# Performance work log

Hardware: AMD Instinct MI355X
Metric: run time of the kernel (lower is better)

## Reference

```python
import jax, jax.numpy as jnp
import numpy as np

B, S, D, Q = 8, 4096, 1024, 16  # batch, seq, embed_dim, n_qubits==ffn_dim


def setup_inputs() -> dict:
    key = jax.random.key(0)
    k = jax.random.split(key, 5)
    x = jax.random.normal(k[0], (B, S, D), dtype=jnp.float32)
    W1 = jax.random.normal(k[1], (D, Q), dtype=jnp.float32) * 0.02
    b1 = jnp.zeros((Q,), dtype=jnp.float32)
    theta = jax.random.normal(k[2], (Q,), dtype=jnp.float32)
    W2 = jax.random.normal(k[3], (Q, D), dtype=jnp.float32) * 0.02
    b2 = jnp.zeros((D,), dtype=jnp.float32)
    return {"x": x, "W1": W1, "b1": b1, "theta": theta, "W2": W2, "b2": b2}


def reference(x, W1, b1, theta, W2, b2):
    # linear1 + ReLU (dropout is identity in eval mode)
    h = jax.nn.relu(jnp.einsum("bsd,dq->bsq", x, W1) + b1)  # [B,S,Q] angles
    # QLayer: RY(h_i) then RY(theta_i) on wire i from |0>; rotations on the
    # same wire compose additively and <Z> after RY(a)|0> is cos(a), so
    # MeasureAll(PauliZ) == cos(h + theta) per wire (exact, product state).
    z = jnp.cos(h + theta)  # [B,S,Q]
    # linear2
    return jnp.einsum("bsq,qd->bsd", z, W2) + b2
```

## Files before the change

kernel.cpp:

```cpp
#include <hip/hip_runtime.h>
#include <math.h>
#include <stdint.h>

#define ROWS_TOTAL 32768
#define DDIM 1024
#define QDIM 16

typedef __attribute__((ext_vector_type(8))) short bf16x8;
typedef __attribute__((ext_vector_type(4))) float f32x4;

union ABfrag { uint32_t u[4]; bf16x8 v; };

__device__ __forceinline__ uint32_t packhi(uint32_t a, uint32_t b) {
  return __builtin_amdgcn_perm(b, a, 0x07060302u);
}

#define ZTPB 512
#define ZWPB 8
#define ZNBLOCKS (ROWS_TOTAL / 16)

__global__ __launch_bounds__(ZTPB, 4)
void z_kernel(const float* __restrict__ x, const float* __restrict__ W1,
              const float* __restrict__ b1, const float* __restrict__ theta,
              float* __restrict__ z, int zstride) {
  const int t    = threadIdx.x;
  const int lane = t & 63;
  const int wid  = t >> 6;
  const int g    = lane >> 4;
  const int q5   = lane & 15;

  __shared__ __align__(16) float xs[16][DDIM];
  __shared__ __align__(16) float red[ZWPB][64][4];

  const int row0 = blockIdx.x * 16;
  const int kb   = wid * 128;

  const float bq = b1[q5];
  const float tq = theta[q5];

  float wf[4][8];
#pragma unroll
  for (int s = 0; s < 4; ++s) {
    const float* wp = W1 + (size_t)(kb + 32 * s + 4 * g) * QDIM + q5;
#pragma unroll
    for (int j = 0; j < 4; ++j) wf[s][j] = wp[(size_t)j * QDIM];
#pragma unroll
    for (int j = 0; j < 4; ++j) wf[s][4 + j] = wp[(size_t)(16 + j) * QDIM];
  }

  float4 st[8];
  {
    const int rs = 2 * wid;
#pragma unroll
    for (int rr = 0; rr < 2; ++rr) {
      const float* xp = x + (size_t)(row0 + rs + rr) * DDIM;
#pragma unroll
      for (int p = 0; p < 4; ++p)
        st[rr * 4 + p] =
            *reinterpret_cast<const float4*>(xp + 4 * (64 * p + lane));
    }
#pragma unroll
    for (int rr = 0; rr < 2; ++rr) {
      const int r = rs + rr;
#pragma unroll
      for (int p = 0; p < 4; ++p) {
        const int u = 64 * p + lane;
        *reinterpret_cast<float4*>(&xs[r][4 * (u ^ (r & 7))]) =
            st[rr * 4 + p];
      }
    }
  }

  ABfrag bhi[4], blo[4];
#pragma unroll
  for (int s = 0; s < 4; ++s) {
    uint32_t u[8], lo[8];
#pragma unroll
    for (int j = 0; j < 8; ++j) {
      u[j]  = __float_as_uint(wf[s][j]);
      lo[j] = __float_as_uint(wf[s][j] - __uint_as_float(u[j] & 0xFFFF0000u));
    }
    bhi[s].u[0] = packhi(u[0], u[1]);   bhi[s].u[1] = packhi(u[2], u[3]);
    bhi[s].u[2] = packhi(u[4], u[5]);   bhi[s].u[3] = packhi(u[6], u[7]);
    blo[s].u[0] = packhi(lo[0], lo[1]); blo[s].u[1] = packhi(lo[2], lo[3]);
    blo[s].u[2] = packhi(lo[4], lo[5]); blo[s].u[3] = packhi(lo[6], lo[7]);
  }

  __syncthreads();

  const int rr = lane & 15;
  const int ub = 32 * wid;
  float4 a0[4], a1[4];
#pragma unroll
  for (int s = 0; s < 4; ++s) {
    a0[s] = *reinterpret_cast<const float4*>(
        &xs[rr][4 * ((ub + 8 * s + g) ^ (rr & 7))]);
    a1[s] = *reinterpret_cast<const float4*>(
        &xs[rr][4 * ((ub + 8 * s + 4 + g) ^ (rr & 7))]);
  }

  f32x4 acc = {0.f, 0.f, 0.f, 0.f};
#pragma unroll
  for (int s = 0; s < 4; ++s) {
    const float fv[8] = {a0[s].x, a0[s].y, a0[s].z, a0[s].w,
                         a1[s].x, a1[s].y, a1[s].z, a1[s].w};
    uint32_t u[8], lo[8];
#pragma unroll
    for (int j = 0; j < 8; ++j) {
      u[j]  = __float_as_uint(fv[j]);
      lo[j] = __float_as_uint(fv[j] - __uint_as_float(u[j] & 0xFFFF0000u));
    }
    ABfrag ahi, alo;
    ahi.u[0] = packhi(u[0], u[1]);   ahi.u[1] = packhi(u[2], u[3]);
    ahi.u[2] = packhi(u[4], u[5]);   ahi.u[3] = packhi(u[6], u[7]);
    alo.u[0] = packhi(lo[0], lo[1]); alo.u[1] = packhi(lo[2], lo[3]);
    alo.u[2] = packhi(lo[4], lo[5]); alo.u[3] = packhi(lo[6], lo[7]);

    acc = __builtin_amdgcn_mfma_f32_16x16x32_bf16(ahi.v, bhi[s].v, acc, 0, 0, 0);
    acc = __builtin_amdgcn_mfma_f32_16x16x32_bf16(alo.v, bhi[s].v, acc, 0, 0, 0);
    acc = __builtin_amdgcn_mfma_f32_16x16x32_bf16(ahi.v, blo[s].v, acc, 0, 0, 0);
  }

  *reinterpret_cast<f32x4*>(&red[wid][lane][0]) = acc;
  __syncthreads();

  if (wid == 0) {
    f32x4 s0 = *reinterpret_cast<const f32x4*>(&red[0][lane][0]);
#pragma unroll
    for (int w = 1; w < ZWPB; ++w)
      s0 += *reinterpret_cast<const f32x4*>(&red[w][lane][0]);

    const int r0 = g * 4;
#pragma unroll
    for (int i = 0; i < 4; ++i) {
      const float sv = fmaxf(s0[i] + bq, 0.f) + tq;
      z[(size_t)(row0 + r0 + i) * zstride + q5] = __cosf(sv);
    }
  }
}

#define OTPB 256
#define ORPB 16
#define ONBLOCKS (ROWS_TOTAL / ORPB)

__global__ __launch_bounds__(OTPB, 4)
void o_kernel(const float* z, int zstride, const float* __restrict__ W2,
              const float* __restrict__ b2, float* out) {
  const int t   = threadIdx.x;
  const int col = 4 * t;

  float4 w2r[QDIM];
#pragma unroll
  for (int q = 0; q < QDIM; ++q)
    w2r[q] = *reinterpret_cast<const float4*>(W2 + (size_t)q * DDIM + col);
  const float4 bb = *reinterpret_cast<const float4*>(b2 + col);

  const int row0 = blockIdx.x * ORPB;

  const float* zp0 = z + (size_t)row0 * zstride;
  float4 zc0 = *reinterpret_cast<const float4*>(zp0 + 0);
  float4 zc1 = *reinterpret_cast<const float4*>(zp0 + 4);
  float4 zc2 = *reinterpret_cast<const float4*>(zp0 + 8);
  float4 zc3 = *reinterpret_cast<const float4*>(zp0 + 12);

#pragma unroll
  for (int r = 0; r < ORPB; ++r) {
    float4 zn0 = zc0, zn1 = zc1, zn2 = zc2, zn3 = zc3;
    if (r + 1 < ORPB) {
      const float* znp = z + (size_t)(row0 + r + 1) * zstride;
      zn0 = *reinterpret_cast<const float4*>(znp + 0);
      zn1 = *reinterpret_cast<const float4*>(znp + 4);
      zn2 = *reinterpret_cast<const float4*>(znp + 8);
      zn3 = *reinterpret_cast<const float4*>(znp + 12);
    }

    const float zv[16] = {zc0.x, zc0.y, zc0.z, zc0.w,
                          zc1.x, zc1.y, zc1.z, zc1.w,
                          zc2.x, zc2.y, zc2.z, zc2.w,
                          zc3.x, zc3.y, zc3.z, zc3.w};
    float4 acc = bb;
#pragma unroll
    for (int q = 0; q < QDIM; ++q) {
      acc.x = fmaf(zv[q], w2r[q].x, acc.x);
      acc.y = fmaf(zv[q], w2r[q].y, acc.y);
      acc.z = fmaf(zv[q], w2r[q].z, acc.z);
      acc.w = fmaf(zv[q], w2r[q].w, acc.w);
    }
    *reinterpret_cast<float4*>(out + (size_t)(row0 + r) * DDIM + col) = acc;

    zc0 = zn0; zc1 = zn1; zc2 = zn2; zc3 = zn3;
  }
}

extern "C" void kernel_launch(void* const* d_in, const int* in_sizes, int n_in,
                              void* d_out, int out_size, void* d_ws, size_t ws_size,
                              hipStream_t stream) {
  const float* x     = (const float*)d_in[0];
  const float* W1    = (const float*)d_in[1];
  const float* b1    = (const float*)d_in[2];
  const float* theta = (const float*)d_in[3];
  const float* W2    = (const float*)d_in[4];
  const float* b2    = (const float*)d_in[5];
  float* out = (float*)d_out;

  const size_t zbytes = (size_t)ROWS_TOTAL * QDIM * sizeof(float);
  float* zbuf;
  int zstride;
  if (d_ws != nullptr && ws_size >= zbytes) {
    zbuf = (float*)d_ws;
    zstride = QDIM;
  } else {
    zbuf = out;
    zstride = DDIM;
  }

  z_kernel<<<dim3(ZNBLOCKS), dim3(ZTPB), 0, stream>>>(x, W1, b1, theta, zbuf, zstride);
  o_kernel<<<dim3(ONBLOCKS), dim3(OTPB), 0, stream>>>(zbuf, zstride, W2, b2, out);
}
```

Baseline: 52.77 us.

## Fuse z computation and output projection into a single kernel

Merges the two kernels into one: the cosine features for each 16-row tile stay in shared memory and feed the W2 projection inside the same block, with each thread producing two output columns. This removes the global round trip of the intermediate z buffer and one kernel launch. In exchange it adds a block barrier, 32 more registers per thread for W2, and couples the read-heavy and write-heavy phases, so each block's output writes start only after its reduction finishes.

```diff
diff --git a/kernel.cpp b/kernel.cpp
--- a/kernel.cpp
+++ b/kernel.cpp
@@ -15,14 +15,15 @@
   return __builtin_amdgcn_perm(b, a, 0x07060302u);
 }
 
-#define ZTPB 512
-#define ZWPB 8
-#define ZNBLOCKS (ROWS_TOTAL / 16)
+#define TPB 512
+#define WPB 8
+#define NBLOCKS (ROWS_TOTAL / 16)
 
-__global__ __launch_bounds__(ZTPB, 4)
-void z_kernel(const float* __restrict__ x, const float* __restrict__ W1,
-              const float* __restrict__ b1, const float* __restrict__ theta,
-              float* __restrict__ z, int zstride) {
+__global__ __launch_bounds__(TPB, 4)
+void fused_kernel(const float* __restrict__ x, const float* __restrict__ W1,
+                  const float* __restrict__ b1, const float* __restrict__ theta,
+                  const float* __restrict__ W2, const float* __restrict__ b2,
+                  float* __restrict__ out) {
   const int t    = threadIdx.x;
   const int lane = t & 63;
   const int wid  = t >> 6;
@@ -30,7 +31,8 @@
   const int q5   = lane & 15;
 
   __shared__ __align__(16) float xs[16][DDIM];
-  __shared__ __align__(16) float red[ZWPB][64][4];
+  __shared__ __align__(16) float red[WPB][64][4];
+  __shared__ __align__(16) float zs[16][QDIM];
 
   const int row0 = blockIdx.x * 16;
   const int kb   = wid * 128;
@@ -121,74 +123,47 @@
     acc = __builtin_amdgcn_mfma_f32_16x16x32_bf16(ahi.v, blo[s].v, acc, 0, 0, 0);
   }
 
+  float2 w2r[QDIM];
+#pragma unroll
+  for (int q = 0; q < QDIM; ++q)
+    w2r[q] = *reinterpret_cast<const float2*>(W2 + (size_t)q * DDIM + 2 * t);
+  const float2 bb = *reinterpret_cast<const float2*>(b2 + 2 * t);
+
   *reinterpret_cast<f32x4*>(&red[wid][lane][0]) = acc;
   __syncthreads();
 
   if (wid == 0) {
     f32x4 s0 = *reinterpret_cast<const f32x4*>(&red[0][lane][0]);
 #pragma unroll
-    for (int w = 1; w < ZWPB; ++w)
+    for (int w = 1; w < WPB; ++w)
       s0 += *reinterpret_cast<const f32x4*>(&red[w][lane][0]);
 
     const int r0 = g * 4;
 #pragma unroll
     for (int i = 0; i < 4; ++i) {
       const float sv = fmaxf(s0[i] + bq, 0.f) + tq;
-      z[(size_t)(row0 + r0 + i) * zstride + q5] = __cosf(sv);
+      zs[r0 + i][q5] = __cosf(sv);
     }
   }
-}
-
-#define OTPB 256
-#define ORPB 16
-#define ONBLOCKS (ROWS_TOTAL / ORPB)
-
-__global__ __launch_bounds__(OTPB, 4)
-void o_kernel(const float* z, int zstride, const float* __restrict__ W2,
-              const float* __restrict__ b2, float* out) {
-  const int t   = threadIdx.x;
-  const int col = 4 * t;
-
-  float4 w2r[QDIM];
-#pragma unroll
-  for (int q = 0; q < QDIM; ++q)
-    w2r[q] = *reinterpret_cast<const float4*>(W2 + (size_t)q * DDIM + col);
-  const float4 bb = *reinterpret_cast<const float4*>(b2 + col);
-
-  const int row0 = blockIdx.x * ORPB;
-
-  const float* zp0 = z + (size_t)row0 * zstride;
-  float4 zc0 = *reinterpret_cast<const float4*>(zp0 + 0);
-  float4 zc1 = *reinterpret_cast<const float4*>(zp0 + 4);
-  float4 zc2 = *reinterpret_cast<const float4*>(zp0 + 8);
-  float4 zc3 = *reinterpret_cast<const float4*>(zp0 + 12);
+  __syncthreads();
 
 #pragma unroll
-  for (int r = 0; r < ORPB; ++r) {
-    float4 zn0 = zc0, zn1 = zc1, zn2 = zc2, zn3 = zc3;
-    if (r + 1 < ORPB) {
-      const float* znp = z + (size_t)(row0 + r + 1) * zstride;
-      zn0 = *reinterpret_cast<const float4*>(znp + 0);
-      zn1 = *reinterpret_cast<const float4*>(znp + 4);
-      zn2 = *reinterpret_cast<const float4*>(znp + 8);
-      zn3 = *reinterpret_cast<const float4*>(znp + 12);
+  for (int r = 0; r < 16; ++r) {
+    float o0 = bb.x, o1 = bb.y;
+#pragma unroll
+    for (int jb = 0; jb < 4; ++jb) {
+      const float4 zv = *reinterpret_cast<const float4*>(&zs[r][4 * jb]);
+      o0 = fmaf(zv.x, w2r[4 * jb + 0].x, o0);
+      o1 = fmaf(zv.x, w2r[4 * jb + 0].y, o1);
+      o0 = fmaf(zv.y, w2r[4 * jb + 1].x, o0);
+      o1 = fmaf(zv.y, w2r[4 * jb + 1].y, o1);
+      o0 = fmaf(zv.z, w2r[4 * jb + 2].x, o0);
+      o1 = fmaf(zv.z, w2r[4 * jb + 2].y, o1);
+      o0 = fmaf(zv.w, w2r[4 * jb + 3].x, o0);
+      o1 = fmaf(zv.w, w2r[4 * jb + 3].y, o1);
     }
-
-    const float zv[16] = {zc0.x, zc0.y, zc0.z, zc0.w,
-                          zc1.x, zc1.y, zc1.z, zc1.w,
-                          zc2.x, zc2.y, zc2.z, zc2.w,
-                          zc3.x, zc3.y, zc3.z, zc3.w};
-    float4 acc = bb;
-#pragma unroll
-    for (int q = 0; q < QDIM; ++q) {
-      acc.x = fmaf(zv[q], w2r[q].x, acc.x);
-      acc.y = fmaf(zv[q], w2r[q].y, acc.y);
-      acc.z = fmaf(zv[q], w2r[q].z, acc.z);
-      acc.w = fmaf(zv[q], w2r[q].w, acc.w);
-    }
-    *reinterpret_cast<float4*>(out + (size_t)(row0 + r) * DDIM + col) = acc;
-
-    zc0 = zn0; zc1 = zn1; zc2 = zn2; zc3 = zn3;
+    *reinterpret_cast<float2*>(out + (size_t)(row0 + r) * DDIM + 2 * t) =
+        make_float2(o0, o1);
   }
 }
 
@@ -203,17 +178,6 @@
   const float* b2    = (const float*)d_in[5];
   float* out = (float*)d_out;
 
-  const size_t zbytes = (size_t)ROWS_TOTAL * QDIM * sizeof(float);
-  float* zbuf;
-  int zstride;
-  if (d_ws != nullptr && ws_size >= zbytes) {
-    zbuf = (float*)d_ws;
-    zstride = QDIM;
-  } else {
-    zbuf = out;
-    zstride = DDIM;
-  }
-
-  z_kernel<<<dim3(ZNBLOCKS), dim3(ZTPB), 0, stream>>>(x, W1, b1, theta, zbuf, zstride);
-  o_kernel<<<dim3(ONBLOCKS), dim3(OTPB), 0, stream>>>(zbuf, zstride, W2, b2, out);
+  fused_kernel<<<dim3(NBLOCKS), dim3(TPB), 0, stream>>>(x, W1, b1, theta, W2,
+                                                        b2, out);
 }
```

After: 54.28 us. 2.9% more time.
